# Kernel optimization log

Measured on AMD Instinct MI355X. Metric: run time of the kernel, lower is better.

## Reference

```python
import jax, jax.numpy as jnp
import numpy as np


def _moie_block(x, w, b, alpha, activation):
    # x: [B, in], w: [K, in, out], b: [K, out], alpha: [B, K]
    z = jnp.einsum('bi,kio->bko', x, w) + b          # [B, K, out] per-expert outputs
    combined = jnp.einsum('bko,bk->bo', z, alpha)    # alpha-weighted sum over experts
    if activation:
        combined = jax.nn.relu(combined)
    return combined


def setup_inputs() -> dict:
    key = jax.random.key(0)
    ks = jax.random.split(key, 8)
    B, D, K, H = 16384, 512, 8, 512
    s = 0.02  # weight init scale
    return {
        'x': jax.random.normal(ks[0], (B, D), jnp.float32),
        'gate_w': jax.random.normal(ks[1], (D, K), jnp.float32) * s,
        'gate_b': jnp.zeros((K,), jnp.float32),
        'w0': jax.random.normal(ks[2], (K, D, H), jnp.float32) * s,
        'b0': jnp.zeros((K, H), jnp.float32),
        'w1': jax.random.normal(ks[3], (K, H, H), jnp.float32) * s,
        'b1': jnp.zeros((K, H), jnp.float32),
        'w2': jax.random.normal(ks[4], (K, H, H), jnp.float32) * s,
        'b2': jnp.zeros((K, H), jnp.float32),
        'wo': jax.random.normal(ks[5], (K, H, D), jnp.float32) * s,
        'bo': jnp.zeros((K, D), jnp.float32),
    }


def reference(x, gate_w, gate_b, w0, b0, w1, b1, w2, b2, wo, bo):
    # Gating: softmax(Linear(x)) -> alpha [B, K]; same alpha reused at every layer.
    alpha = jax.nn.softmax(x @ gate_w + gate_b, axis=-1)
    # n_blocks=3 hidden MoIE blocks: MoIEBlock (no act) -> ReLU -> Dropout(0, eval=identity)
    h = _moie_block(x, w0, b0, alpha, activation=True)
    h = _moie_block(h, w1, b1, alpha, activation=True)
    h = _moie_block(h, w2, b2, alpha, activation=True)
    # Output MoIEBlock: no activation
    return _moie_block(h, wo, bo, alpha, activation=False)
```

## Files before the change

kernel.cpp:

```cpp
#include <hip/hip_runtime.h>
#include <stdint.h>

typedef _Float16 f16;
typedef _Float16 f16x8 __attribute__((ext_vector_type(8)));
typedef float f32x4 __attribute__((ext_vector_type(4)));

#define NROWS 16384
#define DIM   512
#define NEXP  8
#define BM    256
#define BN    128
#define BK    32
#define NKS   (DIM/BK)
#define WSTRIDE (DIM*DIM)

#define GLOAD16(gp, lp) __builtin_amdgcn_global_load_lds( \
    (const __attribute__((address_space(1))) void*)(gp),  \
    (__attribute__((address_space(3))) void*)(lp), 16, 0, 0)

#define MFMA16(a,b,c) __builtin_amdgcn_mfma_f32_16x16x32_f16(a, b, c, 0, 0, 0)

__global__ __launch_bounds__(256) void convert_w(
    const float* __restrict__ w0, const float* __restrict__ w1,
    const float* __restrict__ w2, const float* __restrict__ wo,
    f16* __restrict__ Wt)
{
    __shared__ float tile[32][33];
    int b  = blockIdx.x;
    int m  = b >> 8;
    int bi = (b >> 4) & 15;
    int bj = b & 15;
    int layer = m >> 3;
    const float* src =
        (layer == 0 ? w0 : layer == 1 ? w1 : layer == 2 ? w2 : wo)
        + (size_t)(m & 7) * DIM * DIM;
    f16* dst = Wt + (size_t)m * DIM * DIM;
    int tx = threadIdx.x & 31, ty = threadIdx.x >> 5;
#pragma unroll
    for (int r = 0; r < 4; ++r)
        tile[ty + 8*r][tx] = src[(size_t)(bi*32 + ty + 8*r) * DIM + bj*32 + tx];
    __syncthreads();
#pragma unroll
    for (int r = 0; r < 4; ++r)
        dst[(size_t)(bj*32 + ty + 8*r) * DIM + bi*32 + tx] = (f16)tile[tx][ty + 8*r];
}

__global__ __launch_bounds__(256) void gate_kernel(
    const float* __restrict__ x, const float* __restrict__ gw,
    const float* __restrict__ gb, float* __restrict__ alpha,
    f16* __restrict__ xh)
{
    int tid = threadIdx.x, lane = tid & 63, wid = tid >> 6;
    int row = blockIdx.x * 4 + wid;
    const float* xr = x + (size_t)row * DIM;
    float acc[8] = {0,0,0,0,0,0,0,0};
    float xv[8];
#pragma unroll
    for (int j = 0; j < 8; ++j) {
        int d = lane + 64*j;
        float v = xr[d];
        xv[j] = v;
        const float4* g = (const float4*)(gw + (size_t)d * 8);
        float4 g0 = g[0], g1 = g[1];
        acc[0] += v*g0.x; acc[1] += v*g0.y; acc[2] += v*g0.z; acc[3] += v*g0.w;
        acc[4] += v*g1.x; acc[5] += v*g1.y; acc[6] += v*g1.z; acc[7] += v*g1.w;
    }
#pragma unroll
    for (int mlane = 32; mlane >= 1; mlane >>= 1) {
#pragma unroll
        for (int k = 0; k < 8; ++k) acc[k] += __shfl_xor(acc[k], mlane, 64);
    }
#pragma unroll
    for (int k = 0; k < 8; ++k) acc[k] += gb[k];
    float mx = acc[0];
#pragma unroll
    for (int k = 1; k < 8; ++k) mx = fmaxf(mx, acc[k]);
    float s = 0.f;
#pragma unroll
    for (int k = 0; k < 8; ++k) { acc[k] = __expf(acc[k] - mx); s += acc[k]; }
    float inv = 1.0f / s;
    if (lane == 0) {
        float4 a0 = {acc[0]*inv, acc[1]*inv, acc[2]*inv, acc[3]*inv};
        float4 a1 = {acc[4]*inv, acc[5]*inv, acc[6]*inv, acc[7]*inv};
        *(float4*)(alpha + (size_t)row*8)     = a0;
        *(float4*)(alpha + (size_t)row*8 + 4) = a1;
    }
#pragma unroll
    for (int j = 0; j < 8; ++j)
        xh[(size_t)row * DIM + lane + 64*j] = (f16)xv[j];
}


#define ESTEP(WAITN, ISSUE, SLOT, EIDX) \
    asm volatile("s_waitcnt vmcnt(" #WAITN ")" ::: "memory"); \
    __builtin_amdgcn_s_barrier(); \
    ISSUE \
    { const f16* Bb = Ball + (SLOT)*4096 + bOff; \
      f16x8 bf0 = *(const f16x8*)(Bb); \
      f16x8 bf1 = *(const f16x8*)(Bb + 16*BK); \
      f16x8 bf2 = *(const f16x8*)(Bb + 32*BK); \
      f16x8 bf3 = *(const f16x8*)(Bb + 48*BK); \
      f16 s0 = salh[0][EIDX], s1 = salh[1][EIDX], s2 = salh[2][EIDX], s3 = salh[3][EIDX]; \
      f16x8 a0 = af0 * (f16x8){s0,s0,s0,s0,s0,s0,s0,s0}; \
      f16x8 a1 = af1 * (f16x8){s1,s1,s1,s1,s1,s1,s1,s1}; \
      f16x8 a2 = af2 * (f16x8){s2,s2,s2,s2,s2,s2,s2,s2}; \
      f16x8 a3 = af3 * (f16x8){s3,s3,s3,s3,s3,s3,s3,s3}; \
      __builtin_amdgcn_s_setprio(1); \
      acc[0][0]=MFMA16(a0,bf0,acc[0][0]); acc[0][1]=MFMA16(a0,bf1,acc[0][1]); \
      acc[0][2]=MFMA16(a0,bf2,acc[0][2]); acc[0][3]=MFMA16(a0,bf3,acc[0][3]); \
      acc[1][0]=MFMA16(a1,bf0,acc[1][0]); acc[1][1]=MFMA16(a1,bf1,acc[1][1]); \
      acc[1][2]=MFMA16(a1,bf2,acc[1][2]); acc[1][3]=MFMA16(a1,bf3,acc[1][3]); \
      acc[2][0]=MFMA16(a2,bf0,acc[2][0]); acc[2][1]=MFMA16(a2,bf1,acc[2][1]); \
      acc[2][2]=MFMA16(a2,bf2,acc[2][2]); acc[2][3]=MFMA16(a2,bf3,acc[2][3]); \
      acc[3][0]=MFMA16(a3,bf0,acc[3][0]); acc[3][1]=MFMA16(a3,bf1,acc[3][1]); \
      acc[3][2]=MFMA16(a3,bf2,acc[3][2]); acc[3][3]=MFMA16(a3,bf3,acc[3][3]); \
      __builtin_amdgcn_s_setprio(0); }

#define LOADAF \
      af0 = *(const f16x8*)(Ab + aOff); \
      af1 = *(const f16x8*)(Ab + aOff + 16*BK); \
      af2 = *(const f16x8*)(Ab + aOff + 32*BK); \
      af3 = *(const f16x8*)(Ab + aOff + 48*BK);

template<int RELU, int OUTF32>
__global__ __launch_bounds__(512, 2) void moie_gemm(
    const f16*  __restrict__ A,
    const f16*  __restrict__ Wt,
    const float* __restrict__ alpha,
    const float* __restrict__ bias,
    f16*  __restrict__ Hout,
    float* __restrict__ Fout)
{
    __shared__ __align__(16) f16 Abuf[2][BM*BK];
    __shared__ __align__(16) f16 Bbuf[4][BN*BK];
    __shared__ float alpha_s[BM*9];
    __shared__ float bias_s[NEXP*BN];

    int bid = blockIdx.x;
    int swz = (bid & 7) * 32 + (bid >> 3);
    int cb = swz >> 6, rb = swz & 63;
    int rowBase = rb * BM, colBase = cb * BN;
    int tid = threadIdx.x, lane = tid & 63, wid = tid >> 6;
    int wm = wid >> 1, wn = wid & 1;

    for (int i = tid; i < BM*NEXP; i += 512)
        alpha_s[(i >> 3)*9 + (i & 7)] = alpha[(size_t)(rowBase + (i >> 3))*8 + (i & 7)];
    for (int i = tid; i < NEXP*BN; i += 512)
        bias_s[i] = bias[(i >> 7)*DIM + colBase + (i & 127)];

    int srow = tid >> 2;
    int sg   = ((tid & 3) ^ (srow & 3)) * 8;
    const f16* aSrc = A  + (size_t)(rowBase + srow) * DIM + sg;
    const f16* bSrc = Wt + (size_t)(colBase + srow) * DIM + sg;
    f16* aD0  = Abuf[0] + tid*8;  f16* aD0b = Abuf[0] + 4096 + tid*8;
    f16* aD1  = Abuf[1] + tid*8;  f16* aD1b = Abuf[1] + 4096 + tid*8;
    f16* bD   = Bbuf[0] + tid*8;
    const f16* Ball = Bbuf[0];

    int kg   = ((lane >> 4) ^ (lane & 3)) * 8;
    int aOff = (wm*64 + (lane & 15)) * BK + kg;
    int bOff = (wn*64 + (lane & 15)) * BK + kg;

    __syncthreads();

    GLOAD16(aSrc, aD0); GLOAD16(aSrc + 128*DIM, aD0b);
    GLOAD16(bSrc,                bD);
    GLOAD16(bSrc +   (size_t)WSTRIDE, bD + 4096);
    GLOAD16(bSrc + 2*(size_t)WSTRIDE, bD + 2*4096);

    f16 salh[4][NEXP];
#pragma unroll
    for (int i = 0; i < 4; ++i) {
        int r = wm*64 + i*16 + (lane & 15);
#pragma unroll
        for (int e = 0; e < NEXP; ++e) salh[i][e] = (f16)alpha_s[r*9 + e];
    }

    f32x4 acc[4][4];
#pragma unroll
    for (int i = 0; i < 4; ++i)
#pragma unroll
        for (int j = 0; j < 4; ++j) acc[i][j] = (f32x4){0.f,0.f,0.f,0.f};

    for (int ss = 0; ss < NKS - 1; ++ss) {
        const f16* Ab = (ss & 1) ? Abuf[1] : Abuf[0];
        f16* an0 = (ss & 1) ? aD0  : aD1;
        f16* an1 = (ss & 1) ? aD0b : aD1b;
        const f16* aN = aSrc + (ss + 1)*BK;
        const f16* bB = bSrc + ss*BK;
        f16x8 af0, af1, af2, af3;
        ESTEP(2, { GLOAD16(bB + 3*(size_t)WSTRIDE, bD + 3*4096);
                   GLOAD16(aN, an0); GLOAD16(aN + 128*DIM, an1);
                   LOADAF }, 0, 0)
        ESTEP(4, { GLOAD16(bB + 4*(size_t)WSTRIDE, bD);          }, 1, 1)
        ESTEP(4, { GLOAD16(bB + 5*(size_t)WSTRIDE, bD + 4096);   }, 2, 2)
        ESTEP(4, { GLOAD16(bB + 6*(size_t)WSTRIDE, bD + 2*4096); }, 3, 3)
        ESTEP(2, { GLOAD16(bB + 7*(size_t)WSTRIDE, bD + 3*4096); }, 0, 4)
        ESTEP(2, { GLOAD16(bB + BK,                       bD);          }, 1, 5)
        ESTEP(2, { GLOAD16(bB + BK +   (size_t)WSTRIDE,   bD + 4096);   }, 2, 6)
        ESTEP(2, { GLOAD16(bB + BK + 2*(size_t)WSTRIDE,   bD + 2*4096); }, 3, 7)
    }
    {
        const f16* Ab = Abuf[1];
        const f16* bB = bSrc + (NKS - 1)*BK;
        f16x8 af0, af1, af2, af3;
        ESTEP(2, { GLOAD16(bB + 3*(size_t)WSTRIDE, bD + 3*4096); LOADAF }, 0, 0)
        ESTEP(2, { GLOAD16(bB + 4*(size_t)WSTRIDE, bD);          }, 1, 1)
        ESTEP(2, { GLOAD16(bB + 5*(size_t)WSTRIDE, bD + 4096);   }, 2, 2)
        ESTEP(2, { GLOAD16(bB + 6*(size_t)WSTRIDE, bD + 2*4096); }, 3, 3)
        ESTEP(2, { GLOAD16(bB + 7*(size_t)WSTRIDE, bD + 3*4096); }, 0, 4)
        ESTEP(2, { }, 1, 5)
        ESTEP(1, { }, 2, 6)
        ESTEP(0, { }, 3, 7)
    }

#pragma unroll
    for (int i = 0; i < 4; ++i)
#pragma unroll
        for (int q = 0; q < 4; ++q) {
            int rloc = wm*64 + i*16 + (lane >> 4)*4 + q;
            size_t row = (size_t)(rowBase + rloc);
#pragma unroll
            for (int j = 0; j < 4; ++j) {
                int cloc = wn*64 + j*16 + (lane & 15);
                float v = acc[i][j][q];
#pragma unroll
                for (int e2 = 0; e2 < NEXP; ++e2)
                    v += alpha_s[rloc*9 + e2] * bias_s[e2*BN + cloc];
                if (RELU) v = fmaxf(v, 0.f);
                if (OUTF32) Fout[row*DIM + colBase + cloc] = v;
                else        Hout[row*DIM + colBase + cloc] = (f16)v;
            }
        }
}

extern "C" void kernel_launch(void* const* d_in, const int* in_sizes, int n_in,
                              void* d_out, int out_size, void* d_ws, size_t ws_size,
                              hipStream_t stream)
{
    const float* x  = (const float*)d_in[0];
    const float* gw = (const float*)d_in[1];
    const float* gb = (const float*)d_in[2];
    const float* w0 = (const float*)d_in[3];
    const float* b0 = (const float*)d_in[4];
    const float* w1 = (const float*)d_in[5];
    const float* b1 = (const float*)d_in[6];
    const float* w2 = (const float*)d_in[7];
    const float* b2 = (const float*)d_in[8];
    const float* wo = (const float*)d_in[9];
    const float* bo = (const float*)d_in[10];
    float* out = (float*)d_out;

    char* ws = (char*)d_ws;
    const size_t wtBytes = (size_t)4 * NEXP * DIM * DIM * sizeof(f16);
    f16*   Wt    = (f16*)ws;
    float* alpha = (float*)(ws + wtBytes);
    f16*   h0    = (f16*)(ws + wtBytes + (size_t)NROWS*NEXP*sizeof(float));
    f16*   h1    = h0 + (size_t)NROWS * DIM;
    const size_t L = (size_t)NEXP * DIM * DIM;

    convert_w<<<8192, 256, 0, stream>>>(w0, w1, w2, wo, Wt);
    gate_kernel<<<NROWS/4, 256, 0, stream>>>(x, gw, gb, alpha, h0);

    moie_gemm<1,0><<<256, 512, 0, stream>>>(h0, Wt,       alpha, b0, h1, nullptr);
    moie_gemm<1,0><<<256, 512, 0, stream>>>(h1, Wt + L,   alpha, b1, h0, nullptr);
    moie_gemm<1,0><<<256, 512, 0, stream>>>(h0, Wt + 2*L, alpha, b2, h1, nullptr);
    moie_gemm<0,1><<<256, 512, 0, stream>>>(h1, Wt + 3*L, alpha, bo, nullptr, out);
}
```

Measured before the change: 325.0 us.

## Software-pipeline LDS B-fragment reads with register double buffering in MoIE GEMM

```diff
diff --git a/kernel.cpp b/kernel.cpp
--- a/kernel.cpp
+++ b/kernel.cpp
@@ -11,7 +11,7 @@
 #define BM    256
 #define BN    128
 #define BK    32
-#define NKS   (DIM/BK)
+#define NKS   16
 #define WSTRIDE (DIM*DIM)
 
 #define GLOAD16(gp, lp) __builtin_amdgcn_global_load_lds( \
@@ -19,6 +19,11 @@
     (__attribute__((address_space(3))) void*)(lp), 16, 0, 0)
 
 #define MFMA16(a,b,c) __builtin_amdgcn_mfma_f32_16x16x32_f16(a, b, c, 0, 0, 0)
+
+#define WAITV(N) asm volatile("s_waitcnt vmcnt(" #N ")" ::: "memory")
+#define LGKM0()  do { asm volatile("s_waitcnt lgkmcnt(0)" ::: "memory"); \
+                      __builtin_amdgcn_sched_barrier(0); } while (0)
+#define BAR()    __builtin_amdgcn_s_barrier()
 
 __global__ __launch_bounds__(256) void convert_w(
     const float* __restrict__ w0, const float* __restrict__ w1,
@@ -91,36 +96,36 @@
 }
 
 
-#define ESTEP(WAITN, ISSUE, SLOT, EIDX) \
-    asm volatile("s_waitcnt vmcnt(" #WAITN ")" ::: "memory"); \
-    __builtin_amdgcn_s_barrier(); \
-    ISSUE \
-    { const f16* Bb = Ball + (SLOT)*4096 + bOff; \
-      f16x8 bf0 = *(const f16x8*)(Bb); \
-      f16x8 bf1 = *(const f16x8*)(Bb + 16*BK); \
-      f16x8 bf2 = *(const f16x8*)(Bb + 32*BK); \
-      f16x8 bf3 = *(const f16x8*)(Bb + 48*BK); \
-      f16 s0 = salh[0][EIDX], s1 = salh[1][EIDX], s2 = salh[2][EIDX], s3 = salh[3][EIDX]; \
-      f16x8 a0 = af0 * (f16x8){s0,s0,s0,s0,s0,s0,s0,s0}; \
-      f16x8 a1 = af1 * (f16x8){s1,s1,s1,s1,s1,s1,s1,s1}; \
-      f16x8 a2 = af2 * (f16x8){s2,s2,s2,s2,s2,s2,s2,s2}; \
-      f16x8 a3 = af3 * (f16x8){s3,s3,s3,s3,s3,s3,s3,s3}; \
-      __builtin_amdgcn_s_setprio(1); \
-      acc[0][0]=MFMA16(a0,bf0,acc[0][0]); acc[0][1]=MFMA16(a0,bf1,acc[0][1]); \
-      acc[0][2]=MFMA16(a0,bf2,acc[0][2]); acc[0][3]=MFMA16(a0,bf3,acc[0][3]); \
-      acc[1][0]=MFMA16(a1,bf0,acc[1][0]); acc[1][1]=MFMA16(a1,bf1,acc[1][1]); \
-      acc[1][2]=MFMA16(a1,bf2,acc[1][2]); acc[1][3]=MFMA16(a1,bf3,acc[1][3]); \
-      acc[2][0]=MFMA16(a2,bf0,acc[2][0]); acc[2][1]=MFMA16(a2,bf1,acc[2][1]); \
-      acc[2][2]=MFMA16(a2,bf2,acc[2][2]); acc[2][3]=MFMA16(a2,bf3,acc[2][3]); \
-      acc[3][0]=MFMA16(a3,bf0,acc[3][0]); acc[3][1]=MFMA16(a3,bf1,acc[3][1]); \
-      acc[3][2]=MFMA16(a3,bf2,acc[3][2]); acc[3][3]=MFMA16(a3,bf3,acc[3][3]); \
-      __builtin_amdgcn_s_setprio(0); }
-
-#define LOADAF \
-      af0 = *(const f16x8*)(Ab + aOff); \
-      af1 = *(const f16x8*)(Ab + aOff + 16*BK); \
-      af2 = *(const f16x8*)(Ab + aOff + 32*BK); \
-      af3 = *(const f16x8*)(Ab + aOff + 48*BK);
+#define READ_BF(B, SLOT) \
+    B##0 = *(const f16x8*)(Ball + (SLOT)*4096 + bOff); \
+    B##1 = *(const f16x8*)(Ball + (SLOT)*4096 + bOff + 512); \
+    B##2 = *(const f16x8*)(Ball + (SLOT)*4096 + bOff + 1024); \
+    B##3 = *(const f16x8*)(Ball + (SLOT)*4096 + bOff + 1536);
+
+#define READ_AF(P) \
+    af0 = *(const f16x8*)((P) + aOff); \
+    af1 = *(const f16x8*)((P) + aOff + 512); \
+    af2 = *(const f16x8*)((P) + aOff + 1024); \
+    af3 = *(const f16x8*)((P) + aOff + 1536);
+
+#define MULS(E) { \
+    f16 s0_ = salh0[E], s1_ = salh1[E], s2_ = salh2[E], s3_ = salh3[E]; \
+    a0 = af0 * (f16x8){s0_,s0_,s0_,s0_,s0_,s0_,s0_,s0_}; \
+    a1 = af1 * (f16x8){s1_,s1_,s1_,s1_,s1_,s1_,s1_,s1_}; \
+    a2 = af2 * (f16x8){s2_,s2_,s2_,s2_,s2_,s2_,s2_,s2_}; \
+    a3 = af3 * (f16x8){s3_,s3_,s3_,s3_,s3_,s3_,s3_,s3_}; }
+
+#define MFMA16x(B) \
+    __builtin_amdgcn_s_setprio(1); \
+    acc[0][0]=MFMA16(a0,B##0,acc[0][0]); acc[0][1]=MFMA16(a0,B##1,acc[0][1]); \
+    acc[0][2]=MFMA16(a0,B##2,acc[0][2]); acc[0][3]=MFMA16(a0,B##3,acc[0][3]); \
+    acc[1][0]=MFMA16(a1,B##0,acc[1][0]); acc[1][1]=MFMA16(a1,B##1,acc[1][1]); \
+    acc[1][2]=MFMA16(a1,B##2,acc[1][2]); acc[1][3]=MFMA16(a1,B##3,acc[1][3]); \
+    acc[2][0]=MFMA16(a2,B##0,acc[2][0]); acc[2][1]=MFMA16(a2,B##1,acc[2][1]); \
+    acc[2][2]=MFMA16(a2,B##2,acc[2][2]); acc[2][3]=MFMA16(a2,B##3,acc[2][3]); \
+    acc[3][0]=MFMA16(a3,B##0,acc[3][0]); acc[3][1]=MFMA16(a3,B##1,acc[3][1]); \
+    acc[3][2]=MFMA16(a3,B##2,acc[3][2]); acc[3][3]=MFMA16(a3,B##3,acc[3][3]); \
+    __builtin_amdgcn_s_setprio(0);
 
 template<int RELU, int OUTF32>
 __global__ __launch_bounds__(512, 2) void moie_gemm(
@@ -149,32 +154,44 @@
         bias_s[i] = bias[(i >> 7)*DIM + colBase + (i & 127)];
 
     int srow = tid >> 2;
-    int sg   = ((tid & 3) ^ (srow & 3)) * 8;
+    int sg   = ((tid & 3) ^ ((srow >> 1) & 3)) * 8;
     const f16* aSrc = A  + (size_t)(rowBase + srow) * DIM + sg;
     const f16* bSrc = Wt + (size_t)(colBase + srow) * DIM + sg;
-    f16* aD0  = Abuf[0] + tid*8;  f16* aD0b = Abuf[0] + 4096 + tid*8;
-    f16* aD1  = Abuf[1] + tid*8;  f16* aD1b = Abuf[1] + 4096 + tid*8;
+    f16* aW0  = Abuf[0] + tid*8;  f16* aW0b = Abuf[0] + 4096 + tid*8;
+    f16* aW1  = Abuf[1] + tid*8;  f16* aW1b = Abuf[1] + 4096 + tid*8;
     f16* bD   = Bbuf[0] + tid*8;
     const f16* Ball = Bbuf[0];
 
-    int kg   = ((lane >> 4) ^ (lane & 3)) * 8;
+    int kg   = ((lane >> 4) ^ (((lane & 15) >> 1) & 3)) * 8;
     int aOff = (wm*64 + (lane & 15)) * BK + kg;
     int bOff = (wn*64 + (lane & 15)) * BK + kg;
 
     __syncthreads();
 
-    GLOAD16(aSrc, aD0); GLOAD16(aSrc + 128*DIM, aD0b);
-    GLOAD16(bSrc,                bD);
+    f16 salh0[NEXP], salh1[NEXP], salh2[NEXP], salh3[NEXP];
+    {
+        int r0 = wm*64 + (lane & 15);
+#pragma unroll
+        for (int e = 0; e < NEXP; ++e) {
+            salh0[e] = (f16)alpha_s[(r0     )*9 + e];
+            salh1[e] = (f16)alpha_s[(r0 + 16)*9 + e];
+            salh2[e] = (f16)alpha_s[(r0 + 32)*9 + e];
+            salh3[e] = (f16)alpha_s[(r0 + 48)*9 + e];
+        }
+    }
+
+    GLOAD16(aSrc, aW0); GLOAD16(aSrc + 128*DIM, aW0b);
+    GLOAD16(bSrc,                     bD);
     GLOAD16(bSrc +   (size_t)WSTRIDE, bD + 4096);
     GLOAD16(bSrc + 2*(size_t)WSTRIDE, bD + 2*4096);
-
-    f16 salh[4][NEXP];
-#pragma unroll
-    for (int i = 0; i < 4; ++i) {
-        int r = wm*64 + i*16 + (lane & 15);
-#pragma unroll
-        for (int e = 0; e < NEXP; ++e) salh[i][e] = (f16)alpha_s[r*9 + e];
-    }
+    GLOAD16(bSrc + 3*(size_t)WSTRIDE, bD + 3*4096);
+
+    f16x8 af0, af1, af2, af3, a0, a1, a2, a3;
+    f16x8 bfA0, bfA1, bfA2, bfA3, bfB0, bfB1, bfB2, bfB3;
+
+    WAITV(3); BAR();
+    READ_BF(bfA, 0);
+    LGKM0();
 
     f32x4 acc[4][4];
 #pragma unroll
@@ -183,35 +200,83 @@
         for (int j = 0; j < 4; ++j) acc[i][j] = (f32x4){0.f,0.f,0.f,0.f};
 
     for (int ss = 0; ss < NKS - 1; ++ss) {
-        const f16* Ab = (ss & 1) ? Abuf[1] : Abuf[0];
-        f16* an0 = (ss & 1) ? aD0  : aD1;
-        f16* an1 = (ss & 1) ? aD0b : aD1b;
-        const f16* aN = aSrc + (ss + 1)*BK;
-        const f16* bB = bSrc + ss*BK;
-        f16x8 af0, af1, af2, af3;
-        ESTEP(2, { GLOAD16(bB + 3*(size_t)WSTRIDE, bD + 3*4096);
-                   GLOAD16(aN, an0); GLOAD16(aN + 128*DIM, an1);
-                   LOADAF }, 0, 0)
-        ESTEP(4, { GLOAD16(bB + 4*(size_t)WSTRIDE, bD);          }, 1, 1)
-        ESTEP(4, { GLOAD16(bB + 5*(size_t)WSTRIDE, bD + 4096);   }, 2, 2)
-        ESTEP(4, { GLOAD16(bB + 6*(size_t)WSTRIDE, bD + 2*4096); }, 3, 3)
-        ESTEP(2, { GLOAD16(bB + 7*(size_t)WSTRIDE, bD + 3*4096); }, 0, 4)
-        ESTEP(2, { GLOAD16(bB + BK,                       bD);          }, 1, 5)
-        ESTEP(2, { GLOAD16(bB + BK +   (size_t)WSTRIDE,   bD + 4096);   }, 2, 6)
-        ESTEP(2, { GLOAD16(bB + BK + 2*(size_t)WSTRIDE,   bD + 2*4096); }, 3, 7)
+        const f16* Ard = (ss & 1) ? Abuf[1] : Abuf[0];
+        f16* an0 = (ss & 1) ? aW0  : aW1;
+        f16* an1 = (ss & 1) ? aW0b : aW1b;
+        const f16* aN  = aSrc + (ss + 1)*BK;
+        const f16* bB  = bSrc + ss*BK;
+        const f16* bBn = bB + BK;
+
+        WAITV(2); BAR();
+        READ_AF(Ard); READ_BF(bfB, 1);
+        GLOAD16(bB + 4*(size_t)WSTRIDE, bD);
+        GLOAD16(aN, an0); GLOAD16(aN + 128*DIM, an1);
+        LGKM0(); MULS(0); MFMA16x(bfA);
+        WAITV(4); BAR();
+        READ_BF(bfA, 2);
+        GLOAD16(bB + 5*(size_t)WSTRIDE, bD + 4096);
+        MULS(1); LGKM0(); MFMA16x(bfB);
+        WAITV(4); BAR();
+        READ_BF(bfB, 3);
+        GLOAD16(bB + 6*(size_t)WSTRIDE, bD + 2*4096);
+        MULS(2); LGKM0(); MFMA16x(bfA);
+        WAITV(4); BAR();
+        READ_BF(bfA, 0);
+        GLOAD16(bB + 7*(size_t)WSTRIDE, bD + 3*4096);
+        MULS(3); LGKM0(); MFMA16x(bfB);
+        WAITV(2); BAR();
+        READ_BF(bfB, 1);
+        GLOAD16(bBn, bD);
+        MULS(4); LGKM0(); MFMA16x(bfA);
+        WAITV(2); BAR();
+        READ_BF(bfA, 2);
+        GLOAD16(bBn + (size_t)WSTRIDE, bD + 4096);
+        MULS(5); LGKM0(); MFMA16x(bfB);
+        WAITV(2); BAR();
+        READ_BF(bfB, 3);
+        GLOAD16(bBn + 2*(size_t)WSTRIDE, bD + 2*4096);
+        MULS(6); LGKM0(); MFMA16x(bfA);
+        WAITV(2); BAR();
+        READ_BF(bfA, 0);
+        GLOAD16(bBn + 3*(size_t)WSTRIDE, bD + 3*4096);
+        MULS(7); LGKM0(); MFMA16x(bfB);
     }
     {
-        const f16* Ab = Abuf[1];
-        const f16* bB = bSrc + (NKS - 1)*BK;
-        f16x8 af0, af1, af2, af3;
-        ESTEP(2, { GLOAD16(bB + 3*(size_t)WSTRIDE, bD + 3*4096); LOADAF }, 0, 0)
-        ESTEP(2, { GLOAD16(bB + 4*(size_t)WSTRIDE, bD);          }, 1, 1)
-        ESTEP(2, { GLOAD16(bB + 5*(size_t)WSTRIDE, bD + 4096);   }, 2, 2)
-        ESTEP(2, { GLOAD16(bB + 6*(size_t)WSTRIDE, bD + 2*4096); }, 3, 3)
-        ESTEP(2, { GLOAD16(bB + 7*(size_t)WSTRIDE, bD + 3*4096); }, 0, 4)
-        ESTEP(2, { }, 1, 5)
-        ESTEP(1, { }, 2, 6)
-        ESTEP(0, { }, 3, 7)
+        const f16* Ard = Abuf[1];
+        const f16* bB  = bSrc + (NKS - 1)*BK;
+        WAITV(2); BAR();
+        READ_AF(Ard); READ_BF(bfB, 1);
+        GLOAD16(bB + 4*(size_t)WSTRIDE, bD);
+        LGKM0(); MULS(0); MFMA16x(bfA);
+
+        WAITV(2); BAR();
+        READ_BF(bfA, 2);
+        GLOAD16(bB + 5*(size_t)WSTRIDE, bD + 4096);
+        MULS(1); LGKM0(); MFMA16x(bfB);
+
+        WAITV(2); BAR();
+        READ_BF(bfB, 3);
+        GLOAD16(bB + 6*(size_t)WSTRIDE, bD + 2*4096);
+        MULS(2); LGKM0(); MFMA16x(bfA);
+
+        WAITV(2); BAR();
+        READ_BF(bfA, 0);
+        GLOAD16(bB + 7*(size_t)WSTRIDE, bD + 3*4096);
+        MULS(3); LGKM0(); MFMA16x(bfB);
+
+        WAITV(2); BAR();
+        READ_BF(bfB, 1);
+        MULS(4); LGKM0(); MFMA16x(bfA);
+
+        WAITV(1); BAR();
+        READ_BF(bfA, 2);
+        MULS(5); LGKM0(); MFMA16x(bfB);
+
+        WAITV(0); BAR();
+        READ_BF(bfB, 3);
+        MULS(6); LGKM0(); MFMA16x(bfA);
+
+        MULS(7); MFMA16x(bfB);
     }
 
 #pragma unroll
```

After: 711.9 us. +119.0%, slower.
